# Optimization experiments

Hardware: AMD Instinct MI355X
Metric: run time of the kernel (lower is better)

The kernel has to match this reference:

```python
import jax, jax.numpy as jnp
import numpy as np

D_MODEL = 1024
N_HEADS = 16
HEAD_DIM = D_MODEL // N_HEADS
BATCH = 4
SEQ = 2048


def setup_inputs() -> dict:
    key = jax.random.key(0)
    k_x, k_wqkv, k_bqkv, k_wo, k_bo = jax.random.split(key, 5)
    x = jax.random.normal(k_x, (BATCH, SEQ, D_MODEL), dtype=jnp.float32)
    # causal mask: True = masked (upper triangle, excluding diagonal)
    mask = jnp.triu(jnp.ones((SEQ, SEQ), dtype=bool), k=1)
    lim = 1.0 / np.sqrt(D_MODEL)
    w_qkv = jax.random.uniform(k_wqkv, (D_MODEL, 3 * D_MODEL), jnp.float32, -lim, lim)
    b_qkv = jax.random.uniform(k_bqkv, (3 * D_MODEL,), jnp.float32, -lim, lim)
    w_out = jax.random.uniform(k_wo, (D_MODEL, D_MODEL), jnp.float32, -lim, lim)
    b_out = jax.random.uniform(k_bo, (D_MODEL,), jnp.float32, -lim, lim)
    return {"x": x, "mask": mask, "w_qkv": w_qkv, "b_qkv": b_qkv,
            "w_out": w_out, "b_out": b_out}


def reference(x, mask, w_qkv, b_qkv, w_out, b_out):
    b, s, _ = x.shape
    scale = HEAD_DIM ** -0.5
    qkv = x @ w_qkv + b_qkv                          # [b, s, 3*d]
    qkv = qkv.reshape(b, s, 3, N_HEADS, HEAD_DIM)
    qkv = jnp.transpose(qkv, (2, 0, 3, 1, 4))        # [3, b, h, s, hd]
    q, k, v = qkv[0], qkv[1], qkv[2]
    attn = jnp.einsum('bhqd,bhkd->bhqk', q, k) * scale
    attn = jnp.where(mask, -jnp.inf, attn)
    attn = jax.nn.softmax(attn, axis=-1)
    out = jnp.einsum('bhqk,bhkd->bhqd', attn, v)     # [b, h, s, hd]
    out = jnp.transpose(out, (0, 2, 1, 3)).reshape(b, s, D_MODEL)
    return out @ w_out + b_out
```

## Files before the change

### kernel.cpp

```cpp
#include <hip/hip_runtime.h>
#include <stdint.h>

typedef unsigned short u16;
typedef __attribute__((ext_vector_type(8))) short short8;
typedef __attribute__((ext_vector_type(4))) float f32x4;
typedef __attribute__((ext_vector_type(16))) float f32x16;

#define DEV static __device__ __forceinline__

#define QSCALE 0.18033688011112042f

DEV float fast_exp2(float x) { return __builtin_amdgcn_exp2f(x); }

DEV float bf2f(u16 u) { union { uint32_t i; float f; } x; x.i = ((uint32_t)u) << 16; return x.f; }
DEV u16 f2bf(float f) {
  union { float f; uint32_t i; } x; x.f = f;
  uint32_t r = x.i + 0x7FFFu + ((x.i >> 16) & 1u);
  return (u16)(r >> 16);
}
DEV uint32_t pk_bf16(float lo, float hi) {
  uint32_t r;
  asm("v_cvt_pk_bf16_f32 %0, %1, %2" : "=v"(r) : "v"(lo), "v"(hi));
  return r;
}

DEV void async_copy16(void* lds_dst, const void* gsrc) {
  typedef __attribute__((address_space(1))) void* gp_t;
  typedef __attribute__((address_space(3))) void* lp_t;
  __builtin_amdgcn_global_load_lds((gp_t)(uintptr_t)gsrc,
                                   (lp_t)(uint32_t)(uintptr_t)lds_dst, 16, 0, 0);
}

DEV void gemm_bt_core(const u16* __restrict__ A, const u16* __restrict__ Bt, int K,
                      int m0, int n0, uint8_t* As, uint8_t* Bs,
                      f32x4 (&acc)[4][4], int wave, int lane, int wm, int wn) {
#pragma unroll
  for (int mt = 0; mt < 4; ++mt)
#pragma unroll
    for (int nt = 0; nt < 4; ++nt)
      acc[mt][nt] = (f32x4){0.f, 0.f, 0.f, 0.f};

  for (int k0 = 0; k0 < K; k0 += 64) {
    __syncthreads();
#pragma unroll
    for (int i = 0; i < 4; ++i) {
      int cb = wave * 256 + i * 64;
      int c  = cb + lane;
      int r  = c >> 3;
      int ks = (c & 7) ^ (r & 7);
      async_copy16(As + cb * 16 + lane * 16, A  + (size_t)(m0 + r) * K + k0 + ks * 8);
      async_copy16(Bs + cb * 16 + lane * 16, Bt + (size_t)(n0 + r) * K + k0 + ks * 8);
    }
    __syncthreads();

    short8 af[2][4], bf_[2][4];
#pragma unroll
    for (int kk = 0; kk < 2; ++kk)
#pragma unroll
      for (int t = 0; t < 4; ++t) {
        int ra = wm + t * 16 + (lane & 15);
        af[kk][t]  = *(const short8*)(As + ra * 128 + (((kk * 4 + (lane >> 4)) ^ (ra & 7)) << 4));
        int rb = wn + t * 16 + (lane & 15);
        bf_[kk][t] = *(const short8*)(Bs + rb * 128 + (((kk * 4 + (lane >> 4)) ^ (rb & 7)) << 4));
      }
#pragma unroll
    for (int kk = 0; kk < 2; ++kk)
#pragma unroll
      for (int mt = 0; mt < 4; ++mt)
#pragma unroll
        for (int nt = 0; nt < 4; ++nt)
          acc[mt][nt] = __builtin_amdgcn_mfma_f32_16x16x32_bf16(af[kk][mt], bf_[kk][nt],
                                                                acc[mt][nt], 0, 0, 0);
  }
}

#define BUF_BYTES 49152

DEV void stage_slot(const u16* __restrict__ A, const u16* __restrict__ Bt,
                    int m0, int n0, int k0, uint8_t* buf, int tid) {
  uint8_t* As = buf;
  uint8_t* Bs = buf + 32768;
#pragma unroll
  for (int i = 0; i < 4; ++i) {
    int c = i * 512 + tid;
    int r = c >> 3;
    int ks = (c & 7) ^ (r & 7);
    async_copy16(As + c * 16, A + (size_t)(m0 + r) * 1024 + k0 + ks * 8);
  }
#pragma unroll
  for (int i = 0; i < 2; ++i) {
    int c = i * 512 + tid;
    int r = c >> 3;
    int ks = (c & 7) ^ (r & 7);
    async_copy16(Bs + c * 16, Bt + (size_t)(n0 + r) * 1024 + k0 + ks * 8);
  }
}

DEV void gemm256_core(const u16* __restrict__ A, const u16* __restrict__ Bt,
                      int m0, int n0, uint8_t* lds,
                      f32x4 (&acc)[4][4], int wave, int lane, int tid) {
  const int wm = (wave >> 1) * 64, wn = (wave & 1) * 64;
#pragma unroll
  for (int mf = 0; mf < 4; ++mf)
#pragma unroll
    for (int nf = 0; nf < 4; ++nf)
      acc[mf][nf] = (f32x4){0.f, 0.f, 0.f, 0.f};

  stage_slot(A, Bt, m0, n0, 0,  lds,             tid);
  stage_slot(A, Bt, m0, n0, 64, lds + BUF_BYTES, tid);
  asm volatile("s_waitcnt vmcnt(6)" ::: "memory");
  __builtin_amdgcn_s_barrier();

#pragma unroll 1
  for (int kt = 0; kt < 16; ++kt) {
    const uint8_t* Ab = lds + (kt & 1) * BUF_BYTES;
    const uint8_t* Bb = Ab + 32768;

    short8 a0[4], b0[4], a1[4], b1[4];
#pragma unroll
    for (int f = 0; f < 4; ++f) {
      int ra = wm + f * 16 + (lane & 15);
      int rb = wn + f * 16 + (lane & 15);
      a0[f] = *(const short8*)(Ab + ra * 128 + (((lane >> 4) ^ (ra & 7)) << 4));
      b0[f] = *(const short8*)(Bb + rb * 128 + (((lane >> 4) ^ (rb & 7)) << 4));
    }
#pragma unroll
    for (int f = 0; f < 4; ++f) {
      int ra = wm + f * 16 + (lane & 15);
      int rb = wn + f * 16 + (lane & 15);
      a1[f] = *(const short8*)(Ab + ra * 128 + (((4 + (lane >> 4)) ^ (ra & 7)) << 4));
      b1[f] = *(const short8*)(Bb + rb * 128 + (((4 + (lane >> 4)) ^ (rb & 7)) << 4));
    }

    asm volatile("s_waitcnt lgkmcnt(8)" ::: "memory");
    __builtin_amdgcn_sched_barrier(0);
    __builtin_amdgcn_s_setprio(1);
#pragma unroll
    for (int mf = 0; mf < 4; ++mf)
#pragma unroll
      for (int nf = 0; nf < 4; ++nf)
        acc[mf][nf] = __builtin_amdgcn_mfma_f32_16x16x32_bf16(a0[mf], b0[nf],
                                                              acc[mf][nf], 0, 0, 0);
    __builtin_amdgcn_s_setprio(0);

    asm volatile("s_waitcnt lgkmcnt(0)" ::: "memory");
    __builtin_amdgcn_sched_barrier(0);
    __builtin_amdgcn_s_barrier();

    if (kt + 2 < 16)
      stage_slot(A, Bt, m0, n0, (kt + 2) * 64, lds + (kt & 1) * BUF_BYTES, tid);

    __builtin_amdgcn_s_setprio(1);
#pragma unroll
    for (int mf = 0; mf < 4; ++mf)
#pragma unroll
      for (int nf = 0; nf < 4; ++nf)
        acc[mf][nf] = __builtin_amdgcn_mfma_f32_16x16x32_bf16(a1[mf], b1[nf],
                                                              acc[mf][nf], 0, 0, 0);
    __builtin_amdgcn_s_setprio(0);

    if (kt + 2 < 16) asm volatile("s_waitcnt vmcnt(6)" ::: "memory");
    else             asm volatile("s_waitcnt vmcnt(0)" ::: "memory");
    __builtin_amdgcn_s_barrier();
  }
}

__global__ __launch_bounds__(256, 2) void k_gemm_qkv(
    const u16* __restrict__ X, const u16* __restrict__ WT, const float* __restrict__ bias,
    u16* __restrict__ Q, u16* __restrict__ Kv, u16* __restrict__ Vt) {
  __shared__ __attribute__((aligned(16))) uint8_t As[16384];
  __shared__ __attribute__((aligned(16))) uint8_t Bs[16384];
  const int lane = threadIdx.x & 63, wave = threadIdx.x >> 6;
  const int wm = (wave >> 1) * 64, wn = (wave & 1) * 64;
  const int m0 = blockIdx.x * 128, n0 = blockIdx.y * 128;
  f32x4 acc[4][4];
  gemm_bt_core(X, WT, 1024, m0, n0, As, Bs, acc, wave, lane, wm, wn);
#pragma unroll
  for (int nt = 0; nt < 4; ++nt) {
    int n = n0 + wn + nt * 16 + (lane & 15);
    float bv = bias[n];
    int which = n >> 10, h = (n >> 6) & 15, hd = n & 63;
    if (which == 2) {
#pragma unroll
      for (int mt = 0; mt < 4; ++mt) {
        int m = m0 + wm + mt * 16 + (lane >> 4) * 4;
        int b = m >> 11, s = m & 2047;
        u16 tmp[4];
#pragma unroll
        for (int rg = 0; rg < 4; ++rg) tmp[rg] = f2bf(acc[mt][nt][rg] + bv);
        *(uint64_t*)(Vt + ((size_t)(b * 16 + h) * 64 + hd) * 2048 + s) = *(const uint64_t*)tmp;
      }
    } else {
      u16* base = (which == 0) ? Q : Kv;
      const float mul = (which == 0) ? QSCALE : 1.0f;
#pragma unroll
      for (int mt = 0; mt < 4; ++mt)
#pragma unroll
        for (int rg = 0; rg < 4; ++rg) {
          int m = m0 + wm + mt * 16 + (lane >> 4) * 4 + rg;
          int b = m >> 11, s = m & 2047;
          base[((size_t)(b * 16 + h) * 2048 + s) * 64 + hd] = f2bf((acc[mt][nt][rg] + bv) * mul);
        }
    }
  }
}

__global__ __launch_bounds__(512, 2) void k_gemm_out(
    const u16* __restrict__ A, const u16* __restrict__ WT, const float* __restrict__ bias,
    float* __restrict__ Out) {
  __shared__ __attribute__((aligned(16))) uint8_t lds[2 * BUF_BYTES];
  const int tid = threadIdx.x, lane = tid & 63, wave = tid >> 6;
  const int wm = (wave >> 1) * 64, wn = (wave & 1) * 64;
  const int m0 = blockIdx.x * 256, n0 = blockIdx.y * 128;
  f32x4 acc[4][4];
  gemm256_core(A, WT, m0, n0, lds, acc, wave, lane, tid);
#pragma unroll
  for (int nf = 0; nf < 4; ++nf) {
    int n = n0 + wn + nf * 16 + (lane & 15);
    float bv = bias[n];
#pragma unroll
    for (int mf = 0; mf < 4; ++mf)
#pragma unroll
      for (int rg = 0; rg < 4; ++rg) {
        int m = m0 + wm + mf * 16 + (lane >> 4) * 4 + rg;
        Out[(size_t)m * 1024 + n] = acc[mf][nf][rg] + bv;
      }
  }
}

__global__ __launch_bounds__(256) void k_prep(
    const float* __restrict__ x, u16* __restrict__ Xb,
    const float* __restrict__ w_qkv, u16* __restrict__ wqkvT,
    const float* __restrict__ w_out, u16* __restrict__ woutT) {
  __shared__ u16 tile[64][72];
  const int bid = blockIdx.x;
  if (bid < 4096) {
    size_t i = (size_t)bid * 256 + threadIdx.x;
    float4 a = *(const float4*)(x + i * 8);
    float4 b = *(const float4*)(x + i * 8 + 4);
    u16 tmp[8] = {f2bf(a.x), f2bf(a.y), f2bf(a.z), f2bf(a.w),
                  f2bf(b.x), f2bf(b.y), f2bf(b.z), f2bf(b.w)};
    *(short8*)(Xb + i * 8) = *(const short8*)tmp;
    return;
  }
  const float* src; u16* dst; int R, C, t;
  if (bid < 4864) { t = bid - 4096; src = w_qkv; dst = wqkvT; R = 1024; C = 3072; }
  else            { t = bid - 4864; src = w_out; dst = woutT; R = 1024; C = 1024; }
  const int tr = (t & 15) * 64, tc = (t >> 4) * 64;
  for (int c = threadIdx.x; c < 1024; c += 256) {
    int r = c >> 4, c4 = (c & 15) * 4;
    float4 v = *(const float4*)(src + (size_t)(tr + r) * C + tc + c4);
    tile[r][c4 + 0] = f2bf(v.x); tile[r][c4 + 1] = f2bf(v.y);
    tile[r][c4 + 2] = f2bf(v.z); tile[r][c4 + 3] = f2bf(v.w);
  }
  __syncthreads();
  for (int c = threadIdx.x; c < 512; c += 256) {
    int oc = c >> 3, r8 = (c & 7) * 8;
    u16 tmp[8];
#pragma unroll
    for (int i = 0; i < 8; ++i) tmp[i] = tile[r8 + i][oc];
    *(short8*)(dst + (size_t)(tc + oc) * R + tr + r8) = *(const short8*)tmp;
  }
}

DEV void stage_tile128(const u16* __restrict__ Kg, const u16* __restrict__ Vg,
                       uint8_t* kb, uint8_t* vb, int t, int tid) {
#pragma unroll
  for (int i = 0; i < 4; ++i) {
    int c = i * 256 + tid;
    int r = c >> 3;
    int ks = (c & 7) ^ (r & 7);
    async_copy16(kb + c * 16, Kg + (size_t)(t * 128 + r) * 64 + ks * 8);
  }
#pragma unroll
  for (int i = 0; i < 4; ++i) {
    int c = i * 256 + tid;
    int r = c >> 4;
    int ks = (c & 15) ^ (r & 7);
    async_copy16(vb + c * 16, Vg + (size_t)r * 2048 + t * 128 + ks * 8);
  }
}

__global__ __launch_bounds__(256, 2) void k_attn(
    const u16* __restrict__ Q, const u16* __restrict__ K,
    const u16* __restrict__ Vt, u16* __restrict__ O) {
  __shared__ __attribute__((aligned(16))) uint8_t kbuf[2][16384];
  __shared__ __attribute__((aligned(16))) uint8_t vbuf[2][16384];
  const int tid = threadIdx.x;
  const int lane = tid & 63;
  const int wave = tid >> 6;
  const int q32 = lane & 31, hv = lane >> 5;
  const float NEG_INF = -__builtin_inff();

  int L = blockIdx.x;
  int bh = (L & 7) * 8 + ((L >> 3) >> 3);
  int pair = (L >> 3) & 7;
  const int b = bh >> 4, h = bh & 15;
  const size_t hb = (size_t)bh * (2048 * 64);
  const u16* Qg = Q + hb;
  const u16* Kg = K + hb;
  const u16* Vg = Vt + hb;

#pragma unroll 1
  for (int which = 0; which < 2; ++which) {
    const int s = which ? (15 - pair) : pair;
    const int nt = s + 1;
    const int qbase = s * 128 + wave * 32;
    const int qg = qbase + q32;

    short8 qf[4];
#pragma unroll
    for (int dblk = 0; dblk < 4; ++dblk)
      qf[dblk] = *(const short8*)(Qg + (size_t)qg * 64 + dblk * 16 + hv * 8);

    f32x16 oacc[2] = {};
    float mrun = NEG_INF, lrun = 0.f;

    stage_tile128(Kg, Vg, kbuf[0], vbuf[0], 0, tid);
    __syncthreads();

#pragma unroll 1
    for (int t = 0; t < nt; ++t) {
      const int cur = t & 1;
      if (t + 1 < nt) stage_tile128(Kg, Vg, kbuf[cur ^ 1], vbuf[cur ^ 1], t + 1, tid);

      const uint8_t* kb = kbuf[cur];
      const uint8_t* vb = vbuf[cur];
      const bool h2 = (t * 128 + 64) <= (qbase + 31);

      float sv[64];
      {
        f32x16 sa0 = {}, sa1 = {};
        __builtin_amdgcn_s_setprio(1);
#pragma unroll
        for (int dblk = 0; dblk < 4; ++dblk) {
          short8 kf0 = *(const short8*)(kb + q32 * 128 + (((dblk * 2 + hv) ^ (q32 & 7)) << 4));
          short8 kf1 = *(const short8*)(kb + (32 + q32) * 128 + (((dblk * 2 + hv) ^ (q32 & 7)) << 4));
          sa0 = __builtin_amdgcn_mfma_f32_32x32x16_bf16(kf0, qf[dblk], sa0, 0, 0, 0);
          sa1 = __builtin_amdgcn_mfma_f32_32x32x16_bf16(kf1, qf[dblk], sa1, 0, 0, 0);
        }
        __builtin_amdgcn_s_setprio(0);
#pragma unroll
        for (int r = 0; r < 16; ++r) { sv[r] = sa0[r]; sv[16 + r] = sa1[r]; }
      }
      if (h2) {
        f32x16 sa2 = {}, sa3 = {};
        __builtin_amdgcn_s_setprio(1);
#pragma unroll
        for (int dblk = 0; dblk < 4; ++dblk) {
          short8 kf2 = *(const short8*)(kb + (64 + q32) * 128 + (((dblk * 2 + hv) ^ (q32 & 7)) << 4));
          short8 kf3 = *(const short8*)(kb + (96 + q32) * 128 + (((dblk * 2 + hv) ^ (q32 & 7)) << 4));
          sa2 = __builtin_amdgcn_mfma_f32_32x32x16_bf16(kf2, qf[dblk], sa2, 0, 0, 0);
          sa3 = __builtin_amdgcn_mfma_f32_32x32x16_bf16(kf3, qf[dblk], sa3, 0, 0, 0);
        }
        __builtin_amdgcn_s_setprio(0);
#pragma unroll
        for (int r = 0; r < 16; ++r) { sv[32 + r] = sa2[r]; sv[48 + r] = sa3[r]; }
      }

      if (t == s) {
#pragma unroll
        for (int r = 0; r < 16; ++r) {
          int kl = (r & 3) + 8 * (r >> 2) + 4 * hv;
          if (t * 128 + kl > qg)      sv[r]      = NEG_INF;
          if (t * 128 + 32 + kl > qg) sv[16 + r] = NEG_INF;
        }
        if (h2) {
#pragma unroll
          for (int r = 0; r < 16; ++r) {
            int kl = (r & 3) + 8 * (r >> 2) + 4 * hv;
            if (t * 128 + 64 + kl > qg) sv[32 + r] = NEG_INF;
            if (t * 128 + 96 + kl > qg) sv[48 + r] = NEG_INF;
          }
        }
      }

      float mloc = fmaxf(sv[0], sv[1]);
#pragma unroll
      for (int r = 2; r < 32; ++r) mloc = fmaxf(mloc, sv[r]);
      if (h2) {
#pragma unroll
        for (int r = 32; r < 64; ++r) mloc = fmaxf(mloc, sv[r]);
      }
      float mtile = fmaxf(mloc, __shfl_xor(mloc, 32, 64));
      if (!__all(mtile <= mrun + 8.f)) {
        float mnew = fmaxf(mrun, mtile);
        float corr = fast_exp2(mrun - mnew);
        mrun = mnew;
        lrun *= corr;
#pragma unroll
        for (int r = 0; r < 16; ++r) { oacc[0][r] *= corr; oacc[1][r] *= corr; }
      }
      float ls = 0.f;
#pragma unroll
      for (int r = 0; r < 32; ++r) { sv[r] = fast_exp2(sv[r] - mrun); ls += sv[r]; }
      if (h2) {
#pragma unroll
        for (int r = 32; r < 64; ++r) { sv[r] = fast_exp2(sv[r] - mrun); ls += sv[r]; }
      }
      ls += __shfl_xor(ls, 32, 64);
      lrun += ls;

      __builtin_amdgcn_s_setprio(1);
#pragma unroll
      for (int ksub = 0; ksub < 4; ++ksub) {
        if (ksub < 2 || h2) {
#pragma unroll
          for (int kb2 = 0; kb2 < 2; ++kb2) {
            const int rb = ksub * 16 + kb2 * 8;
            uint32_t pA = pk_bf16(sv[rb + 0], sv[rb + 1]);
            uint32_t pB = pk_bf16(sv[rb + 2], sv[rb + 3]);
            uint32_t pC = pk_bf16(sv[rb + 4], sv[rb + 5]);
            uint32_t pD = pk_bf16(sv[rb + 6], sv[rb + 7]);
            uint32_t X = hv ? pA : pC;
            uint32_t Y = hv ? pB : pD;
            uint32_t sX = (uint32_t)__shfl_xor((int)X, 32, 64);
            uint32_t sY = (uint32_t)__shfl_xor((int)Y, 32, 64);
            union { uint32_t u[4]; short8 s8; } pu;
            pu.u[0] = hv ? sX : pA;
            pu.u[1] = hv ? sY : pB;
            pu.u[2] = hv ? pC : sX;
            pu.u[3] = hv ? pD : sY;
            const int kblk = ksub * 2 + kb2;
            short8 vf0 = *(const short8*)(vb + q32 * 256 + (((kblk * 2 + hv) ^ (q32 & 7)) << 4));
            short8 vf1 = *(const short8*)(vb + (32 + q32) * 256 + (((kblk * 2 + hv) ^ (q32 & 7)) << 4));
            oacc[0] = __builtin_amdgcn_mfma_f32_32x32x16_bf16(vf0, pu.s8, oacc[0], 0, 0, 0);
            oacc[1] = __builtin_amdgcn_mfma_f32_32x32x16_bf16(vf1, pu.s8, oacc[1], 0, 0, 0);
          }
        }
      }
      __builtin_amdgcn_s_setprio(0);

      __syncthreads();
    }

    float rl = 1.0f / lrun;
    u16* orow = O + ((size_t)(b * 2048 + qg)) * 1024 + h * 64;
#pragma unroll
    for (int dt = 0; dt < 2; ++dt)
#pragma unroll
      for (int g = 0; g < 4; ++g) {
        int dbase = dt * 32 + 8 * g + 4 * hv;
        u16 tmp[4];
#pragma unroll
        for (int j2 = 0; j2 < 4; ++j2) tmp[j2] = f2bf(oacc[dt][4 * g + j2] * rl);
        *(uint64_t*)(orow + dbase) = *(const uint64_t*)tmp;
      }
  }
}

extern "C" void kernel_launch(void* const* d_in, const int* in_sizes, int n_in,
                              void* d_out, int out_size, void* d_ws, size_t ws_size,
                              hipStream_t stream) {
  const float* x     = (const float*)d_in[0];
  const float* w_qkv = (const float*)d_in[2];
  const float* b_qkv = (const float*)d_in[3];
  const float* w_out = (const float*)d_in[4];
  const float* b_out = (const float*)d_in[5];
  float* out = (float*)d_out;
  uint8_t* ws = (uint8_t*)d_ws;

  u16* wqkvT = (u16*)(ws);
  u16* woutT = (u16*)(ws +  6291456);
  u16* Xb    = (u16*)(ws +  8388608);
  u16* Qb    = (u16*)(ws + 25165824);
  u16* Kb    = (u16*)(ws + 41943040);
  u16* Vtb   = (u16*)(ws + 58720256);
  u16* AO    = Xb;

  k_prep<<<dim3(5120), 256, 0, stream>>>(x, Xb, w_qkv, wqkvT, w_out, woutT);
  k_gemm_qkv<<<dim3(64, 24), 256, 0, stream>>>(Xb, wqkvT, b_qkv, Qb, Kb, Vtb);
  k_attn<<<dim3(512), 256, 0, stream>>>(Qb, Kb, Vtb, AO);
  k_gemm_out<<<dim3(32, 8), 512, 0, stream>>>(AO, woutT, b_out, out);
}
```

Before: 149.5 us.

## Double-buffer QKV GEMM with async LDS prefetch and split MFMA phases

Replaces the QKV projection's single-buffered GEMM loop, which synchronises twice per K step, with a double-buffered pipeline modeled on the existing 256-row core. Tiles for step k+2 are prefetched into the alternate LDS slot while MFMAs on the current slot run, and vmcnt/lgkmcnt waits and priority hints interleave loads with compute. LDS use per block doubles to 64 KB, which may limit occupancy at two blocks per CU.

```diff
diff --git a/kernel.cpp b/kernel.cpp
--- a/kernel.cpp
+++ b/kernel.cpp
@@ -31,74 +31,31 @@
                                    (lp_t)(uint32_t)(uintptr_t)lds_dst, 16, 0, 0);
 }
 
-DEV void gemm_bt_core(const u16* __restrict__ A, const u16* __restrict__ Bt, int K,
-                      int m0, int n0, uint8_t* As, uint8_t* Bs,
-                      f32x4 (&acc)[4][4], int wave, int lane, int wm, int wn) {
-#pragma unroll
-  for (int mt = 0; mt < 4; ++mt)
-#pragma unroll
-    for (int nt = 0; nt < 4; ++nt)
-      acc[mt][nt] = (f32x4){0.f, 0.f, 0.f, 0.f};
-
-  for (int k0 = 0; k0 < K; k0 += 64) {
-    __syncthreads();
-#pragma unroll
-    for (int i = 0; i < 4; ++i) {
-      int cb = wave * 256 + i * 64;
-      int c  = cb + lane;
-      int r  = c >> 3;
-      int ks = (c & 7) ^ (r & 7);
-      async_copy16(As + cb * 16 + lane * 16, A  + (size_t)(m0 + r) * K + k0 + ks * 8);
-      async_copy16(Bs + cb * 16 + lane * 16, Bt + (size_t)(n0 + r) * K + k0 + ks * 8);
-    }
-    __syncthreads();
-
-    short8 af[2][4], bf_[2][4];
-#pragma unroll
-    for (int kk = 0; kk < 2; ++kk)
-#pragma unroll
-      for (int t = 0; t < 4; ++t) {
-        int ra = wm + t * 16 + (lane & 15);
-        af[kk][t]  = *(const short8*)(As + ra * 128 + (((kk * 4 + (lane >> 4)) ^ (ra & 7)) << 4));
-        int rb = wn + t * 16 + (lane & 15);
-        bf_[kk][t] = *(const short8*)(Bs + rb * 128 + (((kk * 4 + (lane >> 4)) ^ (rb & 7)) << 4));
-      }
-#pragma unroll
-    for (int kk = 0; kk < 2; ++kk)
-#pragma unroll
-      for (int mt = 0; mt < 4; ++mt)
-#pragma unroll
-        for (int nt = 0; nt < 4; ++nt)
-          acc[mt][nt] = __builtin_amdgcn_mfma_f32_16x16x32_bf16(af[kk][mt], bf_[kk][nt],
-                                                                acc[mt][nt], 0, 0, 0);
-  }
-}
-
-#define BUF_BYTES 49152
-
-DEV void stage_slot(const u16* __restrict__ A, const u16* __restrict__ Bt,
-                    int m0, int n0, int k0, uint8_t* buf, int tid) {
+#define G1_BUF 32768
+
+DEV void stage128(const u16* __restrict__ A, const u16* __restrict__ Bt,
+                  int m0, int n0, int k0, uint8_t* buf, int tid) {
   uint8_t* As = buf;
-  uint8_t* Bs = buf + 32768;
+  uint8_t* Bs = buf + 16384;
 #pragma unroll
   for (int i = 0; i < 4; ++i) {
-    int c = i * 512 + tid;
+    int c = i * 256 + tid;
     int r = c >> 3;
     int ks = (c & 7) ^ (r & 7);
     async_copy16(As + c * 16, A + (size_t)(m0 + r) * 1024 + k0 + ks * 8);
   }
 #pragma unroll
-  for (int i = 0; i < 2; ++i) {
-    int c = i * 512 + tid;
+  for (int i = 0; i < 4; ++i) {
+    int c = i * 256 + tid;
     int r = c >> 3;
     int ks = (c & 7) ^ (r & 7);
     async_copy16(Bs + c * 16, Bt + (size_t)(n0 + r) * 1024 + k0 + ks * 8);
   }
 }
 
-DEV void gemm256_core(const u16* __restrict__ A, const u16* __restrict__ Bt,
-                      int m0, int n0, uint8_t* lds,
-                      f32x4 (&acc)[4][4], int wave, int lane, int tid) {
+DEV void gemm128p_core(const u16* __restrict__ A, const u16* __restrict__ Bt,
+                       int m0, int n0, uint8_t* lds,
+                       f32x4 (&acc)[4][4], int wave, int lane, int tid) {
   const int wm = (wave >> 1) * 64, wn = (wave & 1) * 64;
 #pragma unroll
   for (int mf = 0; mf < 4; ++mf)
@@ -106,15 +63,15 @@
     for (int nf = 0; nf < 4; ++nf)
       acc[mf][nf] = (f32x4){0.f, 0.f, 0.f, 0.f};
 
-  stage_slot(A, Bt, m0, n0, 0,  lds,             tid);
-  stage_slot(A, Bt, m0, n0, 64, lds + BUF_BYTES, tid);
-  asm volatile("s_waitcnt vmcnt(6)" ::: "memory");
+  stage128(A, Bt, m0, n0, 0,  lds,          tid);
+  stage128(A, Bt, m0, n0, 64, lds + G1_BUF, tid);
+  asm volatile("s_waitcnt vmcnt(8)" ::: "memory");
   __builtin_amdgcn_s_barrier();
 
 #pragma unroll 1
   for (int kt = 0; kt < 16; ++kt) {
-    const uint8_t* Ab = lds + (kt & 1) * BUF_BYTES;
-    const uint8_t* Bb = Ab + 32768;
+    const uint8_t* Ab = lds + (kt & 1) * G1_BUF;
+    const uint8_t* Bb = Ab + 16384;
 
     short8 a0[4], b0[4], a1[4], b1[4];
 #pragma unroll
@@ -148,7 +105,7 @@
     __builtin_amdgcn_s_barrier();
 
     if (kt + 2 < 16)
-      stage_slot(A, Bt, m0, n0, (kt + 2) * 64, lds + (kt & 1) * BUF_BYTES, tid);
+      stage128(A, Bt, m0, n0, (kt + 2) * 64, lds + (kt & 1) * G1_BUF, tid);
 
     __builtin_amdgcn_s_setprio(1);
 #pragma unroll
@@ -159,6 +116,97 @@
                                                               acc[mf][nf], 0, 0, 0);
     __builtin_amdgcn_s_setprio(0);
 
+    if (kt + 2 < 16) asm volatile("s_waitcnt vmcnt(8)" ::: "memory");
+    else             asm volatile("s_waitcnt vmcnt(0)" ::: "memory");
+    __builtin_amdgcn_s_barrier();
+  }
+}
+
+#define BUF_BYTES 49152
+
+DEV void stage_slot(const u16* __restrict__ A, const u16* __restrict__ Bt,
+                    int m0, int n0, int k0, uint8_t* buf, int tid) {
+  uint8_t* As = buf;
+  uint8_t* Bs = buf + 32768;
+#pragma unroll
+  for (int i = 0; i < 4; ++i) {
+    int c = i * 512 + tid;
+    int r = c >> 3;
+    int ks = (c & 7) ^ (r & 7);
+    async_copy16(As + c * 16, A + (size_t)(m0 + r) * 1024 + k0 + ks * 8);
+  }
+#pragma unroll
+  for (int i = 0; i < 2; ++i) {
+    int c = i * 512 + tid;
+    int r = c >> 3;
+    int ks = (c & 7) ^ (r & 7);
+    async_copy16(Bs + c * 16, Bt + (size_t)(n0 + r) * 1024 + k0 + ks * 8);
+  }
+}
+
+DEV void gemm256_core(const u16* __restrict__ A, const u16* __restrict__ Bt,
+                      int m0, int n0, uint8_t* lds,
+                      f32x4 (&acc)[4][4], int wave, int lane, int tid) {
+  const int wm = (wave >> 1) * 64, wn = (wave & 1) * 64;
+#pragma unroll
+  for (int mf = 0; mf < 4; ++mf)
+#pragma unroll
+    for (int nf = 0; nf < 4; ++nf)
+      acc[mf][nf] = (f32x4){0.f, 0.f, 0.f, 0.f};
+
+  stage_slot(A, Bt, m0, n0, 0,  lds,             tid);
+  stage_slot(A, Bt, m0, n0, 64, lds + BUF_BYTES, tid);
+  asm volatile("s_waitcnt vmcnt(6)" ::: "memory");
+  __builtin_amdgcn_s_barrier();
+
+#pragma unroll 1
+  for (int kt = 0; kt < 16; ++kt) {
+    const uint8_t* Ab = lds + (kt & 1) * BUF_BYTES;
+    const uint8_t* Bb = Ab + 32768;
+
+    short8 a0[4], b0[4], a1[4], b1[4];
+#pragma unroll
+    for (int f = 0; f < 4; ++f) {
+      int ra = wm + f * 16 + (lane & 15);
+      int rb = wn + f * 16 + (lane & 15);
+      a0[f] = *(const short8*)(Ab + ra * 128 + (((lane >> 4) ^ (ra & 7)) << 4));
+      b0[f] = *(const short8*)(Bb + rb * 128 + (((lane >> 4) ^ (rb & 7)) << 4));
+    }
+#pragma unroll
+    for (int f = 0; f < 4; ++f) {
+      int ra = wm + f * 16 + (lane & 15);
+      int rb = wn + f * 16 + (lane & 15);
+      a1[f] = *(const short8*)(Ab + ra * 128 + (((4 + (lane >> 4)) ^ (ra & 7)) << 4));
+      b1[f] = *(const short8*)(Bb + rb * 128 + (((4 + (lane >> 4)) ^ (rb & 7)) << 4));
+    }
+
+    asm volatile("s_waitcnt lgkmcnt(8)" ::: "memory");
+    __builtin_amdgcn_sched_barrier(0);
+    __builtin_amdgcn_s_setprio(1);
+#pragma unroll
+    for (int mf = 0; mf < 4; ++mf)
+#pragma unroll
+      for (int nf = 0; nf < 4; ++nf)
+        acc[mf][nf] = __builtin_amdgcn_mfma_f32_16x16x32_bf16(a0[mf], b0[nf],
+                                                              acc[mf][nf], 0, 0, 0);
+    __builtin_amdgcn_s_setprio(0);
+
+    asm volatile("s_waitcnt lgkmcnt(0)" ::: "memory");
+    __builtin_amdgcn_sched_barrier(0);
+    __builtin_amdgcn_s_barrier();
+
+    if (kt + 2 < 16)
+      stage_slot(A, Bt, m0, n0, (kt + 2) * 64, lds + (kt & 1) * BUF_BYTES, tid);
+
+    __builtin_amdgcn_s_setprio(1);
+#pragma unroll
+    for (int mf = 0; mf < 4; ++mf)
+#pragma unroll
+      for (int nf = 0; nf < 4; ++nf)
+        acc[mf][nf] = __builtin_amdgcn_mfma_f32_16x16x32_bf16(a1[mf], b1[nf],
+                                                              acc[mf][nf], 0, 0, 0);
+    __builtin_amdgcn_s_setprio(0);
+
     if (kt + 2 < 16) asm volatile("s_waitcnt vmcnt(6)" ::: "memory");
     else             asm volatile("s_waitcnt vmcnt(0)" ::: "memory");
     __builtin_amdgcn_s_barrier();
@@ -168,13 +216,12 @@
 __global__ __launch_bounds__(256, 2) void k_gemm_qkv(
     const u16* __restrict__ X, const u16* __restrict__ WT, const float* __restrict__ bias,
     u16* __restrict__ Q, u16* __restrict__ Kv, u16* __restrict__ Vt) {
-  __shared__ __attribute__((aligned(16))) uint8_t As[16384];
-  __shared__ __attribute__((aligned(16))) uint8_t Bs[16384];
-  const int lane = threadIdx.x & 63, wave = threadIdx.x >> 6;
+  __shared__ __attribute__((aligned(16))) uint8_t lds[2 * G1_BUF];
+  const int tid = threadIdx.x, lane = tid & 63, wave = tid >> 6;
   const int wm = (wave >> 1) * 64, wn = (wave & 1) * 64;
   const int m0 = blockIdx.x * 128, n0 = blockIdx.y * 128;
   f32x4 acc[4][4];
-  gemm_bt_core(X, WT, 1024, m0, n0, As, Bs, acc, wave, lane, wm, wn);
+  gemm128p_core(X, WT, m0, n0, lds, acc, wave, lane, tid);
 #pragma unroll
   for (int nt = 0; nt < 4; ++nt) {
     int n = n0 + wn + nt * 16 + (lane & 15);
```

After: 150.4 us. No clear change (+0.6%).
